# Kernel optimization log

Hardware: AMD Instinct MI355X
Metric: run time of the kernel (lower is better)

Reference implementation:

```python
import jax, jax.numpy as jnp
import numpy as np

N_NODES = 100000
N_EDGES = 1600000
N_FEAT = 128
HIDDEN = 128
OUT = 1
NUM_GRAPHS = 2048


def setup_inputs() -> dict:
    key = jax.random.key(0)
    ks = jax.random.split(key, 8)
    x = jax.random.normal(ks[0], (N_NODES, N_FEAT), dtype=jnp.float32)
    edge_index = jax.random.randint(ks[1], (2, N_EDGES), 0, N_NODES, dtype=jnp.int64)
    batch = jnp.sort(jax.random.randint(ks[2], (N_NODES,), 0, NUM_GRAPHS, dtype=jnp.int64))
    s = 1.0 / np.sqrt(N_FEAT)
    W1 = jax.random.normal(ks[3], (N_FEAT, HIDDEN), dtype=jnp.float32) * s
    b1 = jnp.zeros((HIDDEN,), dtype=jnp.float32)
    W2 = jax.random.normal(ks[4], (HIDDEN, HIDDEN), dtype=jnp.float32) * s
    b2 = jnp.zeros((HIDDEN,), dtype=jnp.float32)
    Wlin = jax.random.normal(ks[5], (HIDDEN, OUT), dtype=jnp.float32) * s
    blin = jnp.zeros((OUT,), dtype=jnp.float32)
    return {"x": x, "edge_index": edge_index, "batch": batch,
            "W1": W1, "b1": b1, "W2": W2, "b2": b2, "Wlin": Wlin, "blin": blin}


def gcn_conv(x, W, b, src, dst, n_nodes):
    # PyG GCNConv: x' = D^{-1/2} (A + I) D^{-1/2} (X W) + b, deg includes self-loop
    xw = x @ W  # [N, H]
    deg = jax.ops.segment_sum(jnp.ones(src.shape[0], xw.dtype), dst, num_segments=n_nodes) + 1.0
    dinv = jax.lax.rsqrt(deg)
    norm = dinv[src] * dinv[dst]  # [E]
    agg = jax.ops.segment_sum(xw[src] * norm[:, None], dst, num_segments=n_nodes)
    # self-loop contribution: norm = deg^{-1}
    return agg + xw * (1.0 / deg)[:, None] + b


def global_mean_pool(x, batch, num_graphs):
    sums = jax.ops.segment_sum(x, batch, num_segments=num_graphs)
    cnts = jax.ops.segment_sum(jnp.ones(x.shape[0], x.dtype), batch, num_segments=num_graphs)
    return sums / jnp.maximum(cnts, 1.0)[:, None]


def reference(x, edge_index, batch, W1, b1, W2, b2, Wlin, blin):
    src, dst = edge_index[0], edge_index[1]
    n = x.shape[0]
    h = gcn_conv(x, W1, b1, src, dst, n)
    h = jax.nn.relu(h)  # dropout is a no-op in eval mode
    h = gcn_conv(h, W2, b2, src, dst, n)
    g = global_mean_pool(h, batch, NUM_GRAPHS)  # [G, H]
    return g @ Wlin + blin
```

## Files before the change

kernel.cpp:

```cpp
#include <hip/hip_runtime.h>

#define N_NODES   100000
#define N_EDGES   1600000
#define NFEAT     128
#define NGRAPHS   2048
#define CBSHIFT   8
#define NCB       ((N_NODES + 255) / 256)
#define P1_EPB    8192
#define GEMM_BLOCKS 782
#define BH_BLOCKS   256
#define DP_BLOCKS 100
#define DP_NPB    ((N_NODES + DP_BLOCKS - 1) / DP_BLOCKS)
#define G1_BLOCKS 2048
#define ZCNT      (NGRAPHS + NCB + 64 + 512 + NCB + 1)

typedef __attribute__((ext_vector_type(8))) short short8;
typedef __attribute__((ext_vector_type(4))) float f32x4;

__device__ __forceinline__ unsigned short f2bf(float f) {
    unsigned int u = __float_as_uint(f);
    u += 0x7FFFu + ((u >> 16) & 1u);
    return (unsigned short)(u >> 16);
}

__device__ __forceinline__ void acc8s(float* acc, uint4 v, float s) {
    acc[0] = fmaf(s, __uint_as_float(v.x << 16), acc[0]);
    acc[1] = fmaf(s, __uint_as_float(v.x & 0xFFFF0000u), acc[1]);
    acc[2] = fmaf(s, __uint_as_float(v.y << 16), acc[2]);
    acc[3] = fmaf(s, __uint_as_float(v.y & 0xFFFF0000u), acc[3]);
    acc[4] = fmaf(s, __uint_as_float(v.z << 16), acc[4]);
    acc[5] = fmaf(s, __uint_as_float(v.z & 0xFFFF0000u), acc[5]);
    acc[6] = fmaf(s, __uint_as_float(v.w << 16), acc[6]);
    acc[7] = fmaf(s, __uint_as_float(v.w & 0xFFFF0000u), acc[7]);
}

__global__ __launch_bounds__(256) void k_misc(const float* __restrict__ W1,
                                              unsigned short* __restrict__ WT1,
                                              const float* __restrict__ W2,
                                              const float* __restrict__ Wlin,
                                              const float* __restrict__ b2,
                                              const float* __restrict__ blin,
                                              float* __restrict__ w2l,
                                              int* __restrict__ zeros) {
    const int blk = blockIdx.x;
    const int t = threadIdx.x;
    if (blk < 16) {
        int base = blk * 1024 + t * 4;
        #pragma unroll
        for (int q = 0; q < 4; ++q) {
            int i = base + q;
            int n = i >> 7, k = i & 127;
            WT1[i] = f2bf(W1[k * 128 + n]);
        }
    } else if (blk == 16) {
        __shared__ float s[256];
        int i = t >> 1, half = t & 1;
        float ps = 0.f;
        for (int j = half * 64; j < half * 64 + 64; ++j)
            ps += W2[i * 128 + j] * Wlin[j];
        s[t] = ps;
        __syncthreads();
        if (!half) w2l[i] = s[t] + s[t + 1];
        __syncthreads();
        float pc = (t < 128) ? b2[t] * Wlin[t] : 0.f;
        s[t] = pc;
        __syncthreads();
        for (int off = 128; off > 0; off >>= 1) {
            if (t < off) s[t] += s[t + off];
            __syncthreads();
        }
        if (t == 0) w2l[128] = s[0] + blin[0];
    } else {
        int i = (blk - 17) * 256 + t;
        if (i < ZCNT) zeros[i] = 0;
    }
}

__global__ __launch_bounds__(256) void k_gemm_bhist(const float* __restrict__ X,
                                                    const unsigned short* __restrict__ WT,
                                                    unsigned short* __restrict__ C,
                                                    const int* __restrict__ dst,
                                                    int* __restrict__ bcount) {
    if (blockIdx.x >= GEMM_BLOCKS) {
        __shared__ int h[NCB];
        for (int i = threadIdx.x; i < NCB; i += 256) h[i] = 0;
        __syncthreads();
        int b = blockIdx.x - GEMM_BLOCKS;
        int stride = BH_BLOCKS * 256;
        for (int e = b * 256 + threadIdx.x; e < N_EDGES; e += stride)
            atomicAdd(&h[dst[e] >> CBSHIFT], 1);
        __syncthreads();
        for (int i = threadIdx.x; i < NCB; i += 256) {
            int v = h[i];
            if (v) atomicAdd(&bcount[i], v);
        }
        return;
    }
    const int tid  = threadIdx.x;
    const int R0   = blockIdx.x * 128;
    const int wv   = tid >> 6;
    const int lane = tid & 63;
    const int m16  = lane & 15;
    const int quad = lane >> 4;
    const int r0 = R0 + wv * 32 + m16;
    const int r1 = r0 + 16;
    const bool ok0 = r0 < N_NODES, ok1 = r1 < N_NODES;

    f32x4 acc[2][8] = {};
    #pragma unroll
    for (int ks = 0; ks < 4; ++ks) {
        const int k0 = ks * 32 + quad * 8;
        short8 a0 = {}, a1 = {};
        if (ok0) {
            float4 f0 = *(const float4*)(X + (size_t)r0 * NFEAT + k0);
            float4 f1 = *(const float4*)(X + (size_t)r0 * NFEAT + k0 + 4);
            a0[0] = (short)f2bf(f0.x); a0[1] = (short)f2bf(f0.y);
            a0[2] = (short)f2bf(f0.z); a0[3] = (short)f2bf(f0.w);
            a0[4] = (short)f2bf(f1.x); a0[5] = (short)f2bf(f1.y);
            a0[6] = (short)f2bf(f1.z); a0[7] = (short)f2bf(f1.w);
        }
        if (ok1) {
            float4 f0 = *(const float4*)(X + (size_t)r1 * NFEAT + k0);
            float4 f1 = *(const float4*)(X + (size_t)r1 * NFEAT + k0 + 4);
            a1[0] = (short)f2bf(f0.x); a1[1] = (short)f2bf(f0.y);
            a1[2] = (short)f2bf(f0.z); a1[3] = (short)f2bf(f0.w);
            a1[4] = (short)f2bf(f1.x); a1[5] = (short)f2bf(f1.y);
            a1[6] = (short)f2bf(f1.z); a1[7] = (short)f2bf(f1.w);
        }
        #pragma unroll
        for (int ct = 0; ct < 8; ++ct) {
            short8 bb = *(const short8*)(WT + (ct * 16 + m16) * 128 + k0);
            acc[0][ct] = __builtin_amdgcn_mfma_f32_16x16x32_bf16(a0, bb, acc[0][ct], 0, 0, 0);
            acc[1][ct] = __builtin_amdgcn_mfma_f32_16x16x32_bf16(a1, bb, acc[1][ct], 0, 0, 0);
        }
    }
    #pragma unroll
    for (int t2 = 0; t2 < 2; ++t2) {
        int rbase = R0 + wv * 32 + t2 * 16 + quad * 4;
        #pragma unroll
        for (int reg = 0; reg < 4; ++reg) {
            int gr = rbase + reg;
            if (gr < N_NODES) {
                #pragma unroll
                for (int ct = 0; ct < 8; ++ct)
                    C[(size_t)gr * NFEAT + ct * 16 + m16] = f2bf(acc[t2][ct][reg]);
            }
        }
    }
}

__global__ __launch_bounds__(256) void k_p1(const int* __restrict__ src,
                                            const int* __restrict__ dst,
                                            const int* __restrict__ bcount,
                                            int* __restrict__ bstart,
                                            int* __restrict__ alloc,
                                            unsigned int* __restrict__ pairs) {
    __shared__ int hist[NCB], base[NCB], cur[NCB], bst[NCB], s[256];
    const int t = threadIdx.x;
    for (int i = t; i < NCB; i += 256) { hist[i] = 0; cur[i] = 0; }
    int v0 = (2 * t < NCB) ? bcount[2 * t] : 0;
    int v1 = (2 * t + 1 < NCB) ? bcount[2 * t + 1] : 0;
    int local = v0 + v1;
    s[t] = local;
    __syncthreads();
    for (int off = 1; off < 256; off <<= 1) {
        int x = (t >= off) ? s[t - off] : 0;
        __syncthreads();
        s[t] += x;
        __syncthreads();
    }
    int excl = s[t] - local;
    if (2 * t < NCB)     bst[2 * t] = excl;
    if (2 * t + 1 < NCB) bst[2 * t + 1] = excl + v0;
    if (blockIdx.x == 0) {
        if (2 * t < NCB)     bstart[2 * t] = excl;
        if (2 * t + 1 < NCB) bstart[2 * t + 1] = excl + v0;
        if (t == 255) bstart[NCB] = s[255];
    }
    __syncthreads();
    const int e0 = blockIdx.x * P1_EPB;
    const int e1 = min(e0 + P1_EPB, N_EDGES);
    for (int e = e0 + t; e < e1; e += 256)
        atomicAdd(&hist[dst[e] >> CBSHIFT], 1);
    __syncthreads();
    const int off0 = (blockIdx.x * 89) % NCB;
    for (int k = t; k < NCB; k += 256) {
        int i = k + off0;
        if (i >= NCB) i -= NCB;
        int c = hist[i];
        base[i] = c ? (bst[i] + atomicAdd(&alloc[i], c)) : 0;
    }
    __syncthreads();
    for (int e = e0 + t; e < e1; e += 256) {
        int d = dst[e];
        int b = d >> CBSHIFT;
        int r = atomicAdd(&cur[b], 1);
        pairs[base[b] + r] = (unsigned int)src[e] | ((unsigned int)(d & 255) << 17);
    }
}

__global__ __launch_bounds__(256) void k_p2(const unsigned int* __restrict__ pairs,
                                            const int* __restrict__ bstart,
                                            int* __restrict__ csr_src,
                                            int* __restrict__ row_start,
                                            int* __restrict__ indeg,
                                            float* __restrict__ dinv,
                                            int* __restrict__ dcount) {
    __shared__ int hist[256], sst[256], cur[256], s[256], dh[64];
    const int b = blockIdx.x;
    const int t = threadIdx.x;
    const int beg = bstart[b];
    const int end = bstart[b + 1];
    hist[t] = 0; cur[t] = 0;
    if (t < 64) dh[t] = 0;
    __syncthreads();
    for (int i = beg + t; i < end; i += 256)
        atomicAdd(&hist[pairs[i] >> 17], 1);
    __syncthreads();
    int v = hist[t];
    s[t] = v;
    __syncthreads();
    for (int off = 1; off < 256; off <<= 1) {
        int x = (t >= off) ? s[t - off] : 0;
        __syncthreads();
        s[t] += x;
        __syncthreads();
    }
    sst[t] = s[t] - v;
    __syncthreads();
    {
        int node = (b << CBSHIFT) + t;
        if (node < N_NODES) {
            row_start[node] = beg + sst[t];
            indeg[node] = v;
            dinv[node] = rsqrtf((float)v + 1.0f);
            atomicAdd(&dh[63 - min(v, 63)], 1);
        }
    }
    for (int i = beg + t; i < end; i += 256) {
        unsigned int pv = pairs[i];
        int dl = pv >> 17;
        int r = atomicAdd(&cur[dl], 1);
        csr_src[beg + sst[dl] + r] = (int)(pv & 0x1FFFFu);
    }
    __syncthreads();
    if (t < 64 && dh[t]) atomicAdd(&dcount[((b & 7) << 6) + t], dh[t]);
}

__global__ __launch_bounds__(256) void k_dperm(const int* __restrict__ indeg,
                                               const int* __restrict__ row_start,
                                               const float* __restrict__ dinv,
                                               const int* __restrict__ dcount,
                                               int* __restrict__ dalloc,
                                               int4* __restrict__ meta) {
    __shared__ int h[64], base[64], cur[64], s[64];
    const int t = threadIdx.x;
    int v = 0;
    if (t < 64) {
        h[t] = 0; cur[t] = 0;
        #pragma unroll
        for (int sh = 0; sh < 8; ++sh) v += dcount[(sh << 6) + t];
        s[t] = v;
    }
    __syncthreads();
    for (int off = 1; off < 64; off <<= 1) {
        int x = (t >= off && t < 64) ? s[t - off] : 0;
        __syncthreads();
        if (t < 64) s[t] += x;
        __syncthreads();
    }
    int myst = (t < 64) ? s[t] - v : 0;
    const int i0 = blockIdx.x * DP_NPB;
    const int i1 = min(i0 + DP_NPB, N_NODES);
    for (int i = i0 + t; i < i1; i += 256)
        atomicAdd(&h[63 - min(indeg[i], 63)], 1);
    __syncthreads();
    if (t < 64) {
        int c = h[t];
        base[t] = c ? (myst + atomicAdd(&dalloc[t], c)) : 0;
    }
    __syncthreads();
    for (int i = i0 + t; i < i1; i += 256) {
        int dg = indeg[i];
        int bin = 63 - min(dg, 63);
        int r = atomicAdd(&cur[bin], 1);
        meta[base[bin] + r] = make_int4(row_start[i], dg, __float_as_int(dinv[i]), i);
    }
}

__global__ __launch_bounds__(256) void k_gather1(const unsigned short* __restrict__ xwb,
                                                 const int* __restrict__ csr_src,
                                                 const float* __restrict__ dinv,
                                                 const float* __restrict__ b,
                                                 const float* __restrict__ w2l,
                                                 const int4* __restrict__ meta,
                                                 float* __restrict__ z) {
    const int t     = threadIdx.x;
    const int lane  = t & 63;
    const int p     = lane & 15;
    const int gbase = lane & 48;
    const int j0    = p & 7;
    const int ngroups = G1_BLOCKS * 16;
    int gid = blockIdx.x * 16 + (t >> 4);
    const uint4* tab = (const uint4*)xwb;
    float4 b0 = *(const float4*)(b + p * 8);
    float4 b1 = *(const float4*)(b + p * 8 + 4);
    float4 w0 = *(const float4*)(w2l + p * 8);
    float4 w1 = *(const float4*)(w2l + p * 8 + 4);

    for (int nidx = gid; nidx < N_NODES; nidx += ngroups) {
        const int4 md = meta[nidx];
        const int beg   = md.x;
        const int cnt   = md.y;
        const float dvn = __int_as_float(md.z);
        const int node  = md.w;
        float acc[8] = {};
        acc8s(acc, tab[(size_t)node * 16 + p], dvn);
        const int nch = (cnt + 7) >> 3;
        if (nch) {
            int myA; float dvA; uint4 vA[8];
            int myB; float dvB; uint4 vB[8];
            {
                bool vld = j0 < cnt;
                int jj = vld ? j0 : 0;
                int sld = csr_src[beg + jj];
                myA = vld ? sld : node;
                float dv = dinv[myA];
                dvA = vld ? dv : 0.f;
                #pragma unroll
                for (int q = 0; q < 8; ++q) {
                    int idx = __shfl(myA, gbase + q);
                    vA[q] = tab[(size_t)idx * 16 + p];
                }
            }
            int c = 0;
            for (;;) {
                const bool hb = (c + 1 < nch);
                if (hb) {
                    int j = (c + 1) * 8 + j0;
                    bool vld = j < cnt;
                    int jj = vld ? j : 0;
                    int sld = csr_src[beg + jj];
                    myB = vld ? sld : node;
                    float dv = dinv[myB];
                    dvB = vld ? dv : 0.f;
                    #pragma unroll
                    for (int q = 0; q < 8; ++q) {
                        int idx = __shfl(myB, gbase + q);
                        vB[q] = tab[(size_t)idx * 16 + p];
                    }
                }
                #pragma unroll
                for (int q = 0; q < 8; ++q) {
                    float sv = __shfl(dvA, gbase + q);
                    acc8s(acc, vA[q], sv);
                }
                ++c;
                if (!hb) break;
                const bool ha = (c + 1 < nch);
                if (ha) {
                    int j = (c + 1) * 8 + j0;
                    bool vld = j < cnt;
                    int jj = vld ? j : 0;
                    int sld = csr_src[beg + jj];
                    myA = vld ? sld : node;
                    float dv = dinv[myA];
                    dvA = vld ? dv : 0.f;
                    #pragma unroll
                    for (int q = 0; q < 8; ++q) {
                        int idx = __shfl(myA, gbase + q);
                        vA[q] = tab[(size_t)idx * 16 + p];
                    }
                }
                #pragma unroll
                for (int q = 0; q < 8; ++q) {
                    float sv = __shfl(dvB, gbase + q);
                    acc8s(acc, vB[q], sv);
                }
                ++c;
                if (!ha) break;
            }
        }
        float s = fmaxf(acc[0] * dvn + b0.x, 0.f) * w0.x
                + fmaxf(acc[1] * dvn + b0.y, 0.f) * w0.y
                + fmaxf(acc[2] * dvn + b0.z, 0.f) * w0.z
                + fmaxf(acc[3] * dvn + b0.w, 0.f) * w0.w
                + fmaxf(acc[4] * dvn + b1.x, 0.f) * w1.x
                + fmaxf(acc[5] * dvn + b1.y, 0.f) * w1.y
                + fmaxf(acc[6] * dvn + b1.z, 0.f) * w1.z
                + fmaxf(acc[7] * dvn + b1.w, 0.f) * w1.w;
        s += __shfl_xor(s, 1);
        s += __shfl_xor(s, 2);
        s += __shfl_xor(s, 4);
        s += __shfl_xor(s, 8);
        if (p == 0) z[node] = s * dvn;
    }
}

__global__ __launch_bounds__(256) void k_gather2s(const float* __restrict__ z,
                                                  const int* __restrict__ csr_src,
                                                  const int4* __restrict__ meta,
                                                  const int* __restrict__ batch,
                                                  float* __restrict__ gsum) {
    int tid = blockIdx.x * blockDim.x + threadIdx.x;
    int nidx = tid >> 2;
    int q = tid & 3;
    if (nidx >= N_NODES) return;
    int4 md = meta[nidx];
    const int beg = md.x, cnt = md.y, node = md.w;
    const float dvn = __int_as_float(md.z);
    float a = (q == 0) ? z[node] : 0.f;
    for (int j = q; j < cnt; j += 4)
        a += z[csr_src[beg + j]];
    a += __shfl_xor(a, 1);
    a += __shfl_xor(a, 2);
    if (q == 0) atomicAdd(&gsum[batch[node]], a * dvn);
}

__global__ void k_final(const float* __restrict__ gsum, const int* __restrict__ batch,
                        const float* __restrict__ c2, float* __restrict__ out) {
    int g = blockIdx.x * blockDim.x + threadIdx.x;
    if (g >= NGRAPHS) return;
    int lo = 0, hi = N_NODES;
    while (lo < hi) { int m = (lo + hi) >> 1; if (batch[m] < g) lo = m + 1; else hi = m; }
    int lb = lo;
    lo = 0; hi = N_NODES;
    int g1 = g + 1;
    while (lo < hi) { int m = (lo + hi) >> 1; if (batch[m] < g1) lo = m + 1; else hi = m; }
    float cnt = (float)(lo - lb);
    out[g] = gsum[g] / fmaxf(cnt, 1.0f) + c2[0];
}

extern "C" void kernel_launch(void* const* d_in, const int* in_sizes, int n_in,
                              void* d_out, int out_size, void* d_ws, size_t ws_size,
                              hipStream_t stream) {
    const float* x    = (const float*)d_in[0];
    const int*   ei   = (const int*)d_in[1];
    const int*   bat  = (const int*)d_in[2];
    const float* W1   = (const float*)d_in[3];
    const float* b1   = (const float*)d_in[4];
    const float* W2   = (const float*)d_in[5];
    const float* b2   = (const float*)d_in[6];
    const float* Wlin = (const float*)d_in[7];
    const float* blin = (const float*)d_in[8];
    float* out = (float*)d_out;

    const int* src = ei;
    const int* dst = ei + N_EDGES;

    const size_t NF = (size_t)N_NODES * NFEAT;
    unsigned short* bufA = (unsigned short*)d_ws;
    float* z       = (float*)(bufA + NF);
    float* dinv    = z + N_NODES;
    int* row_start = (int*)(dinv + N_NODES);
    int* indeg     = row_start + N_NODES;
    int* bstart    = indeg + N_NODES;
    float* gsum    = (float*)(bstart + NCB + 1);
    int* alloc     = (int*)(gsum + NGRAPHS);
    int* dalloc    = alloc + NCB;
    int* dcount    = dalloc + 64;
    int* bcount    = dcount + 512;
    int* ctr       = bcount + NCB;
    unsigned short* WT1 = (unsigned short*)(ctr + 1);
    float* w2l     = (float*)(WT1 + 128 * 128);
    unsigned int* pairs = (unsigned int*)(w2l + 132);
    int* csr_src   = (int*)(pairs + N_EDGES);
    int4* meta     = (int4*)(((size_t)pairs + 15) & ~(size_t)15);

    const int BS = 256;
    int p1_blocks   = (N_EDGES + P1_EPB - 1) / P1_EPB;
    int g2_blocks   = (4 * N_NODES + BS - 1) / BS;
    int misc_blocks = 17 + (ZCNT + BS - 1) / BS;

    k_misc<<<misc_blocks, BS, 0, stream>>>(W1, WT1, W2, Wlin, b2, blin, w2l, (int*)gsum);
    k_gemm_bhist<<<GEMM_BLOCKS + BH_BLOCKS, BS, 0, stream>>>(x, WT1, bufA, dst, bcount);

    k_p1<<<p1_blocks, BS, 0, stream>>>(src, dst, bcount, bstart, alloc, pairs);
    k_p2<<<NCB, BS, 0, stream>>>(pairs, bstart, csr_src, row_start, indeg, dinv, dcount);
    k_dperm<<<DP_BLOCKS, BS, 0, stream>>>(indeg, row_start, dinv, dcount, dalloc, meta);

    k_gather1<<<G1_BLOCKS, BS, 0, stream>>>(bufA, csr_src, dinv, b1, w2l, meta, z);

    k_gather2s<<<g2_blocks, BS, 0, stream>>>(z, csr_src, meta, bat, gsum);

    k_final<<<(NGRAPHS + BS - 1) / BS, BS, 0, stream>>>(gsum, bat, w2l + 128, out);
}
```

Before: 278.3 us.

## Split GEMM across preprocessing kernels, drop global degree sort, fuse final reduction

```diff
diff --git a/kernel.cpp b/kernel.cpp
--- a/kernel.cpp
+++ b/kernel.cpp
@@ -7,12 +7,15 @@
 #define CBSHIFT   8
 #define NCB       ((N_NODES + 255) / 256)
 #define P1_EPB    8192
+#define P1_BLOCKS ((N_EDGES + P1_EPB - 1) / P1_EPB)
 #define GEMM_BLOCKS 782
+#define GEMM_HALF   391
 #define BH_BLOCKS   256
-#define DP_BLOCKS 100
-#define DP_NPB    ((N_NODES + DP_BLOCKS - 1) / DP_BLOCKS)
 #define G1_BLOCKS 2048
-#define ZCNT      (NGRAPHS + NCB + 64 + 512 + NCB + 1)
+#define G2_BLOCKS ((4 * N_NODES + 255) / 256)
+#define ZCNT      (NGRAPHS + NCB + NCB + 1)
+#define ZB        ((ZCNT + 255) / 256)
+#define MISC_BLOCKS (17 + ZB + 8)
 
 typedef __attribute__((ext_vector_type(8))) short short8;
 typedef __attribute__((ext_vector_type(4))) float f32x4;
@@ -34,70 +37,11 @@
     acc[7] = fmaf(s, __uint_as_float(v.w & 0xFFFF0000u), acc[7]);
 }
 
-__global__ __launch_bounds__(256) void k_misc(const float* __restrict__ W1,
-                                              unsigned short* __restrict__ WT1,
-                                              const float* __restrict__ W2,
-                                              const float* __restrict__ Wlin,
-                                              const float* __restrict__ b2,
-                                              const float* __restrict__ blin,
-                                              float* __restrict__ w2l,
-                                              int* __restrict__ zeros) {
-    const int blk = blockIdx.x;
-    const int t = threadIdx.x;
-    if (blk < 16) {
-        int base = blk * 1024 + t * 4;
-        #pragma unroll
-        for (int q = 0; q < 4; ++q) {
-            int i = base + q;
-            int n = i >> 7, k = i & 127;
-            WT1[i] = f2bf(W1[k * 128 + n]);
-        }
-    } else if (blk == 16) {
-        __shared__ float s[256];
-        int i = t >> 1, half = t & 1;
-        float ps = 0.f;
-        for (int j = half * 64; j < half * 64 + 64; ++j)
-            ps += W2[i * 128 + j] * Wlin[j];
-        s[t] = ps;
-        __syncthreads();
-        if (!half) w2l[i] = s[t] + s[t + 1];
-        __syncthreads();
-        float pc = (t < 128) ? b2[t] * Wlin[t] : 0.f;
-        s[t] = pc;
-        __syncthreads();
-        for (int off = 128; off > 0; off >>= 1) {
-            if (t < off) s[t] += s[t + off];
-            __syncthreads();
-        }
-        if (t == 0) w2l[128] = s[0] + blin[0];
-    } else {
-        int i = (blk - 17) * 256 + t;
-        if (i < ZCNT) zeros[i] = 0;
-    }
-}
-
-__global__ __launch_bounds__(256) void k_gemm_bhist(const float* __restrict__ X,
-                                                    const unsigned short* __restrict__ WT,
-                                                    unsigned short* __restrict__ C,
-                                                    const int* __restrict__ dst,
-                                                    int* __restrict__ bcount) {
-    if (blockIdx.x >= GEMM_BLOCKS) {
-        __shared__ int h[NCB];
-        for (int i = threadIdx.x; i < NCB; i += 256) h[i] = 0;
-        __syncthreads();
-        int b = blockIdx.x - GEMM_BLOCKS;
-        int stride = BH_BLOCKS * 256;
-        for (int e = b * 256 + threadIdx.x; e < N_EDGES; e += stride)
-            atomicAdd(&h[dst[e] >> CBSHIFT], 1);
-        __syncthreads();
-        for (int i = threadIdx.x; i < NCB; i += 256) {
-            int v = h[i];
-            if (v) atomicAdd(&bcount[i], v);
-        }
-        return;
-    }
-    const int tid  = threadIdx.x;
-    const int R0   = blockIdx.x * 128;
+__device__ __forceinline__ void gemm_tile(const float* __restrict__ X,
+                                          const unsigned short* __restrict__ WT,
+                                          unsigned short* __restrict__ C,
+                                          int gblk, int tid) {
+    const int R0   = gblk * 128;
     const int wv   = tid >> 6;
     const int lane = tid & 63;
     const int m16  = lane & 15;
@@ -149,12 +93,96 @@
     }
 }
 
-__global__ __launch_bounds__(256) void k_p1(const int* __restrict__ src,
-                                            const int* __restrict__ dst,
-                                            const int* __restrict__ bcount,
-                                            int* __restrict__ bstart,
-                                            int* __restrict__ alloc,
-                                            unsigned int* __restrict__ pairs) {
+__global__ __launch_bounds__(256) void k_misc(const float* __restrict__ W1,
+                                              unsigned short* __restrict__ WT1,
+                                              const float* __restrict__ W2,
+                                              const float* __restrict__ Wlin,
+                                              const float* __restrict__ b2,
+                                              const float* __restrict__ blin,
+                                              float* __restrict__ w2l,
+                                              int* __restrict__ zeros,
+                                              const int* __restrict__ batch,
+                                              float* __restrict__ cntf) {
+    const int blk = blockIdx.x;
+    const int t = threadIdx.x;
+    if (blk < 16) {
+        int base = blk * 1024 + t * 4;
+        #pragma unroll
+        for (int q = 0; q < 4; ++q) {
+            int i = base + q;
+            int n = i >> 7, k = i & 127;
+            WT1[i] = f2bf(W1[k * 128 + n]);
+        }
+    } else if (blk == 16) {
+        __shared__ float s[256];
+        int i = t >> 1, half = t & 1;
+        float ps = 0.f;
+        for (int j = half * 64; j < half * 64 + 64; ++j)
+            ps += W2[i * 128 + j] * Wlin[j];
+        s[t] = ps;
+        __syncthreads();
+        if (!half) w2l[i] = s[t] + s[t + 1];
+        __syncthreads();
+        float pc = (t < 128) ? b2[t] * Wlin[t] : 0.f;
+        s[t] = pc;
+        __syncthreads();
+        for (int off = 128; off > 0; off >>= 1) {
+            if (t < off) s[t] += s[t + off];
+            __syncthreads();
+        }
+        if (t == 0) w2l[128] = s[0] + blin[0];
+    } else if (blk < 17 + ZB) {
+        int i = (blk - 17) * 256 + t;
+        if (i < ZCNT) zeros[i] = 0;
+    } else {
+        int g = (blk - (17 + ZB)) * 256 + t;
+        int lo = 0, hi = N_NODES;
+        while (lo < hi) { int m = (lo + hi) >> 1; if (batch[m] < g) lo = m + 1; else hi = m; }
+        int lb = lo;
+        lo = 0; hi = N_NODES;
+        int g1 = g + 1;
+        while (lo < hi) { int m = (lo + hi) >> 1; if (batch[m] < g1) lo = m + 1; else hi = m; }
+        cntf[g] = fmaxf((float)(lo - lb), 1.0f);
+    }
+}
+
+__global__ __launch_bounds__(256) void k_gA_bhist(const float* __restrict__ X,
+                                                  const unsigned short* __restrict__ WT,
+                                                  unsigned short* __restrict__ C,
+                                                  const int* __restrict__ dst,
+                                                  int* __restrict__ bcount) {
+    if (blockIdx.x < GEMM_HALF) {
+        gemm_tile(X, WT, C, blockIdx.x, threadIdx.x);
+        return;
+    }
+    __shared__ int h[NCB];
+    for (int i = threadIdx.x; i < NCB; i += 256) h[i] = 0;
+    __syncthreads();
+    int b = blockIdx.x - GEMM_HALF;
+    int stride = BH_BLOCKS * 256;
+    for (int e = b * 256 + threadIdx.x; e < N_EDGES; e += stride)
+        atomicAdd(&h[dst[e] >> CBSHIFT], 1);
+    __syncthreads();
+    for (int i = threadIdx.x; i < NCB; i += 256) {
+        int v = h[i];
+        if (v) atomicAdd(&bcount[i], v);
+    }
+}
+
+__global__ __launch_bounds__(256) void k_gB_p1(const float* __restrict__ X,
+                                               const unsigned short* __restrict__ WT,
+                                               unsigned short* __restrict__ C,
+                                               const int* __restrict__ src,
+                                               const int* __restrict__ dst,
+                                               const int* __restrict__ bcount,
+                                               int* __restrict__ bstart,
+                                               int* __restrict__ alloc,
+                                               unsigned int* __restrict__ pairs) {
+    if (blockIdx.x < GEMM_HALF) {
+        gemm_tile(X, WT, C, blockIdx.x + GEMM_HALF, threadIdx.x);
+        return;
+    }
+    const int b = blockIdx.x - GEMM_HALF;
     __shared__ int hist[NCB], base[NCB], cur[NCB], bst[NCB], s[256];
     const int t = threadIdx.x;
     for (int i = t; i < NCB; i += 256) { hist[i] = 0; cur[i] = 0; }
@@ -172,18 +200,18 @@
     int excl = s[t] - local;
     if (2 * t < NCB)     bst[2 * t] = excl;
     if (2 * t + 1 < NCB) bst[2 * t + 1] = excl + v0;
-    if (blockIdx.x == 0) {
+    if (b == 0) {
         if (2 * t < NCB)     bstart[2 * t] = excl;
         if (2 * t + 1 < NCB) bstart[2 * t + 1] = excl + v0;
         if (t == 255) bstart[NCB] = s[255];
     }
     __syncthreads();
-    const int e0 = blockIdx.x * P1_EPB;
+    const int e0 = b * P1_EPB;
     const int e1 = min(e0 + P1_EPB, N_EDGES);
     for (int e = e0 + t; e < e1; e += 256)
         atomicAdd(&hist[dst[e] >> CBSHIFT], 1);
     __syncthreads();
-    const int off0 = (blockIdx.x * 89) % NCB;
+    const int off0 = (b * 89) % NCB;
     for (int k = t; k < NCB; k += 256) {
         int i = k + off0;
         if (i >= NCB) i -= NCB;
@@ -193,26 +221,24 @@
     __syncthreads();
     for (int e = e0 + t; e < e1; e += 256) {
         int d = dst[e];
-        int b = d >> CBSHIFT;
-        int r = atomicAdd(&cur[b], 1);
-        pairs[base[b] + r] = (unsigned int)src[e] | ((unsigned int)(d & 255) << 17);
+        int bb = d >> CBSHIFT;
+        int r = atomicAdd(&cur[bb], 1);
+        pairs[base[bb] + r] = (unsigned int)src[e] | ((unsigned int)(d & 255) << 17);
     }
 }
 
 __global__ __launch_bounds__(256) void k_p2(const unsigned int* __restrict__ pairs,
                                             const int* __restrict__ bstart,
                                             int* __restrict__ csr_src,
-                                            int* __restrict__ row_start,
-                                            int* __restrict__ indeg,
                                             float* __restrict__ dinv,
-                                            int* __restrict__ dcount) {
-    __shared__ int hist[256], sst[256], cur[256], s[256], dh[64];
+                                            int4* __restrict__ meta) {
+    __shared__ int hist[256], sst[256], cur[256], s[256], dh[64], dhc[64];
     const int b = blockIdx.x;
     const int t = threadIdx.x;
     const int beg = bstart[b];
     const int end = bstart[b + 1];
     hist[t] = 0; cur[t] = 0;
-    if (t < 64) dh[t] = 0;
+    if (t < 64) { dh[t] = 0; dhc[t] = 0; }
     __syncthreads();
     for (int i = beg + t; i < end; i += 256)
         atomicAdd(&hist[pairs[i] >> 17], 1);
@@ -228,14 +254,11 @@
     }
     sst[t] = s[t] - v;
     __syncthreads();
-    {
-        int node = (b << CBSHIFT) + t;
-        if (node < N_NODES) {
-            row_start[node] = beg + sst[t];
-            indeg[node] = v;
-            dinv[node] = rsqrtf((float)v + 1.0f);
-            atomicAdd(&dh[63 - min(v, 63)], 1);
-        }
+    const int node = (b << CBSHIFT) + t;
+    const bool valid = node < N_NODES;
+    if (valid) {
+        dinv[node] = rsqrtf((float)v + 1.0f);
+        atomicAdd(&dh[63 - min(v, 63)], 1);
     }
     for (int i = beg + t; i < end; i += 256) {
         unsigned int pv = pairs[i];
@@ -244,24 +267,7 @@
         csr_src[beg + sst[dl] + r] = (int)(pv & 0x1FFFFu);
     }
     __syncthreads();
-    if (t < 64 && dh[t]) atomicAdd(&dcount[((b & 7) << 6) + t], dh[t]);
-}
-
-__global__ __launch_bounds__(256) void k_dperm(const int* __restrict__ indeg,
-                                               const int* __restrict__ row_start,
-                                               const float* __restrict__ dinv,
-                                               const int* __restrict__ dcount,
-                                               int* __restrict__ dalloc,
-                                               int4* __restrict__ meta) {
-    __shared__ int h[64], base[64], cur[64], s[64];
-    const int t = threadIdx.x;
-    int v = 0;
-    if (t < 64) {
-        h[t] = 0; cur[t] = 0;
-        #pragma unroll
-        for (int sh = 0; sh < 8; ++sh) v += dcount[(sh << 6) + t];
-        s[t] = v;
-    }
+    if (t < 64) s[t] = dh[t];
     __syncthreads();
     for (int off = 1; off < 64; off <<= 1) {
         int x = (t >= off && t < 64) ? s[t - off] : 0;
@@ -269,22 +275,12 @@
         if (t < 64) s[t] += x;
         __syncthreads();
     }
-    int myst = (t < 64) ? s[t] - v : 0;
-    const int i0 = blockIdx.x * DP_NPB;
-    const int i1 = min(i0 + DP_NPB, N_NODES);
-    for (int i = i0 + t; i < i1; i += 256)
-        atomicAdd(&h[63 - min(indeg[i], 63)], 1);
-    __syncthreads();
-    if (t < 64) {
-        int c = h[t];
-        base[t] = c ? (myst + atomicAdd(&dalloc[t], c)) : 0;
-    }
-    __syncthreads();
-    for (int i = i0 + t; i < i1; i += 256) {
-        int dg = indeg[i];
-        int bin = 63 - min(dg, 63);
-        int r = atomicAdd(&cur[bin], 1);
-        meta[base[bin] + r] = make_int4(row_start[i], dg, __float_as_int(dinv[i]), i);
+    if (valid) {
+        int bin = 63 - min(v, 63);
+        int r = atomicAdd(&dhc[bin], 1);
+        int rank = s[bin] - dh[bin] + r;
+        meta[(b << CBSHIFT) + rank] =
+            make_int4(beg + sst[t], v, __float_as_int(rsqrtf((float)v + 1.0f)), node);
     }
 }
 
@@ -397,38 +393,42 @@
     }
 }
 
-__global__ __launch_bounds__(256) void k_gather2s(const float* __restrict__ z,
-                                                  const int* __restrict__ csr_src,
-                                                  const int4* __restrict__ meta,
-                                                  const int* __restrict__ batch,
-                                                  float* __restrict__ gsum) {
-    int tid = blockIdx.x * blockDim.x + threadIdx.x;
+__global__ __launch_bounds__(256) void k_g2fin(const float* __restrict__ z,
+                                               const int* __restrict__ csr_src,
+                                               const int4* __restrict__ meta,
+                                               const int* __restrict__ batch,
+                                               float* __restrict__ gsum,
+                                               int* __restrict__ done,
+                                               const float* __restrict__ cntf,
+                                               const float* __restrict__ c2v,
+                                               float* __restrict__ out) {
+    const int t = threadIdx.x;
+    int tid = blockIdx.x * 256 + t;
     int nidx = tid >> 2;
     int q = tid & 3;
-    if (nidx >= N_NODES) return;
-    int4 md = meta[nidx];
-    const int beg = md.x, cnt = md.y, node = md.w;
-    const float dvn = __int_as_float(md.z);
-    float a = (q == 0) ? z[node] : 0.f;
-    for (int j = q; j < cnt; j += 4)
-        a += z[csr_src[beg + j]];
-    a += __shfl_xor(a, 1);
-    a += __shfl_xor(a, 2);
-    if (q == 0) atomicAdd(&gsum[batch[node]], a * dvn);
-}
-
-__global__ void k_final(const float* __restrict__ gsum, const int* __restrict__ batch,
-                        const float* __restrict__ c2, float* __restrict__ out) {
-    int g = blockIdx.x * blockDim.x + threadIdx.x;
-    if (g >= NGRAPHS) return;
-    int lo = 0, hi = N_NODES;
-    while (lo < hi) { int m = (lo + hi) >> 1; if (batch[m] < g) lo = m + 1; else hi = m; }
-    int lb = lo;
-    lo = 0; hi = N_NODES;
-    int g1 = g + 1;
-    while (lo < hi) { int m = (lo + hi) >> 1; if (batch[m] < g1) lo = m + 1; else hi = m; }
-    float cnt = (float)(lo - lb);
-    out[g] = gsum[g] / fmaxf(cnt, 1.0f) + c2[0];
+    if (nidx < N_NODES) {
+        int4 md = meta[nidx];
+        const int beg = md.x, cnt = md.y, node = md.w;
+        const float dvn = __int_as_float(md.z);
+        float a = (q == 0) ? z[node] : 0.f;
+        for (int j = q; j < cnt; j += 4)
+            a += z[csr_src[beg + j]];
+        a += __shfl_xor(a, 1);
+        a += __shfl_xor(a, 2);
+        if (q == 0) atomicAdd(&gsum[batch[node]], a * dvn);
+    }
+    __threadfence();
+    __syncthreads();
+    __shared__ int slast;
+    if (t == 0) slast = (atomicAdd(done, 1) == (int)gridDim.x - 1);
+    __syncthreads();
+    if (slast) {
+        float c2 = c2v[0];
+        for (int g = t; g < NGRAPHS; g += 256) {
+            float gs = atomicAdd(&gsum[g], 0.0f);
+            out[g] = gs / cntf[g] + c2;
+        }
+    }
 }
 
 extern "C" void kernel_launch(void* const* d_in, const int* in_sizes, int n_in,
@@ -452,36 +452,27 @@
     unsigned short* bufA = (unsigned short*)d_ws;
     float* z       = (float*)(bufA + NF);
     float* dinv    = z + N_NODES;
-    int* row_start = (int*)(dinv + N_NODES);
-    int* indeg     = row_start + N_NODES;
-    int* bstart    = indeg + N_NODES;
+    int* bstart    = (int*)(dinv + N_NODES);
     float* gsum    = (float*)(bstart + NCB + 1);
     int* alloc     = (int*)(gsum + NGRAPHS);
-    int* dalloc    = alloc + NCB;
-    int* dcount    = dalloc + 64;
-    int* bcount    = dcount + 512;
-    int* ctr       = bcount + NCB;
-    unsigned short* WT1 = (unsigned short*)(ctr + 1);
+    int* bcount    = alloc + NCB;
+    int* done      = bcount + NCB;
+    float* cntf    = (float*)(done + 1);
+    unsigned short* WT1 = (unsigned short*)(cntf + NGRAPHS);
     float* w2l     = (float*)(WT1 + 128 * 128);
     unsigned int* pairs = (unsigned int*)(w2l + 132);
     int* csr_src   = (int*)(pairs + N_EDGES);
-    int4* meta     = (int4*)(((size_t)pairs + 15) & ~(size_t)15);
+    int4* meta     = (int4*)(((size_t)(csr_src + N_EDGES) + 15) & ~(size_t)15);
 
     const int BS = 256;
-    int p1_blocks   = (N_EDGES + P1_EPB - 1) / P1_EPB;
-    int g2_blocks   = (4 * N_NODES + BS - 1) / BS;
-    int misc_blocks = 17 + (ZCNT + BS - 1) / BS;
-
-    k_misc<<<misc_blocks, BS, 0, stream>>>(W1, WT1, W2, Wlin, b2, blin, w2l, (int*)gsum);
-    k_gemm_bhist<<<GEMM_BLOCKS + BH_BLOCKS, BS, 0, stream>>>(x, WT1, bufA, dst, bcount);
-
-    k_p1<<<p1_blocks, BS, 0, stream>>>(src, dst, bcount, bstart, alloc, pairs);
-    k_p2<<<NCB, BS, 0, stream>>>(pairs, bstart, csr_src, row_start, indeg, dinv, dcount);
-    k_dperm<<<DP_BLOCKS, BS, 0, stream>>>(indeg, row_start, dinv, dcount, dalloc, meta);
-
+
+    k_misc<<<MISC_BLOCKS, BS, 0, stream>>>(W1, WT1, W2, Wlin, b2, blin, w2l,
+                                           (int*)gsum, bat, cntf);
+    k_gA_bhist<<<GEMM_HALF + BH_BLOCKS, BS, 0, stream>>>(x, WT1, bufA, dst, bcount);
+    k_gB_p1<<<GEMM_HALF + P1_BLOCKS, BS, 0, stream>>>(x, WT1, bufA, src, dst, bcount,
+                                                      bstart, alloc, pairs);
+    k_p2<<<NCB, BS, 0, stream>>>(pairs, bstart, csr_src, dinv, meta);
     k_gather1<<<G1_BLOCKS, BS, 0, stream>>>(bufA, csr_src, dinv, b1, w2l, meta, z);
-
-    k_gather2s<<<g2_blocks, BS, 0, stream>>>(z, csr_src, meta, bat, gsum);
-
-    k_final<<<(NGRAPHS + BS - 1) / BS, BS, 0, stream>>>(gsum, bat, w2l + 128, out);
-}
+    k_g2fin<<<G2_BLOCKS, BS, 0, stream>>>(z, csr_src, meta, bat, gsum, done, cntf,
+                                          w2l + 128, out);
+}
```

Result: slower. 367.7 us (+32.1%).
